# Performance work log

Measured on AMD Instinct MI355X. Metric: run time of the kernel, lower is better.

## Reference

```python
import jax, jax.numpy as jnp
import numpy as np

B, T, N, F = 8, 32, 10000, 16
E = 160000
HG, HT = 64, 128
EPS = 1e-5


def setup_inputs() -> dict:
    key = jax.random.key(0)
    ks = jax.random.split(key, 12)
    s = lambda i, shape, sc=0.05: jax.random.normal(ks[i], shape, dtype=jnp.float32) * sc
    return {
        "x_seq": jax.random.normal(ks[0], (B, T, N, F), dtype=jnp.float32),
        "edge_index": jax.random.randint(ks[1], (2, E), 0, N),
        "W1l": s(2, (HG, F)), "b1": jnp.zeros((HG,), jnp.float32), "W1r": s(3, (HG, F)),
        "g1": jnp.ones((HG,), jnp.float32), "be1": jnp.zeros((HG,), jnp.float32),
        "W2l": s(4, (HG, HG)), "b2": jnp.zeros((HG,), jnp.float32), "W2r": s(5, (HG, HG)),
        "g2": jnp.ones((HG,), jnp.float32), "be2": jnp.zeros((HG,), jnp.float32),
        "W_ih": s(6, (3 * HT, HG)), "W_hh": s(7, (3 * HT, HT)),
        "b_ih": jnp.zeros((3 * HT,), jnp.float32), "b_hh": jnp.zeros((3 * HT,), jnp.float32),
        "Wh": s(8, (1, HT)), "bh": jnp.zeros((1,), jnp.float32),
    }


def _layernorm(h, g, b):
    mu = h.mean(-1, keepdims=True)
    var = ((h - mu) ** 2).mean(-1, keepdims=True)
    return (h - mu) * jax.lax.rsqrt(var + EPS) * g + b


def reference(x_seq, edge_index, W1l, b1, W1r, g1, be1, W2l, b2, W2r, g2, be2,
              W_ih, W_hh, b_ih, b_hh, Wh, bh):
    src, dst = edge_index[0], edge_index[1]
    deg = jax.ops.segment_sum(jnp.ones((E,), x_seq.dtype), dst, num_segments=N)
    inv_deg = (1.0 / jnp.maximum(deg, 1.0))[:, None]  # [N,1]

    def aggregate(x):  # x: [B,N,F] -> mean over incoming neighbors per node
        msgs = x[:, src, :]  # [B,E,F] gather
        agg = jax.vmap(lambda m: jax.ops.segment_sum(m, dst, num_segments=N))(msgs)
        return agg * inv_deg

    def sage(x, Wl, bl, Wr, g, b):
        # PyG SAGEConv(mean): lin_l(agg) + lin_r(x); then LayerNorm + ReLU (dropout=eval)
        h = aggregate(x) @ Wl.T + bl + x @ Wr.T
        return jax.nn.relu(_layernorm(h, g, b))

    def step(_, xt):  # xt: [B,N,F] -> pooled [B,HG]
        h = sage(xt, W1l, b1, W1r, g1, be1)
        h = sage(h, W2l, b2, W2r, g2, be2)
        return None, h.mean(axis=1)

    _, H = jax.lax.scan(step, None, jnp.swapaxes(x_seq, 0, 1))  # [T,B,HG]

    def gru_step(h, x):  # PyTorch GRU gate order: r, z, n
        gi = x @ W_ih.T + b_ih
        gh = h @ W_hh.T + b_hh
        ir, iz, in_ = jnp.split(gi, 3, axis=-1)
        hr, hz, hn = jnp.split(gh, 3, axis=-1)
        r = jax.nn.sigmoid(ir + hr)
        z = jax.nn.sigmoid(iz + hz)
        n = jnp.tanh(in_ + r * hn)
        return (1.0 - z) * n + z * h, None

    h0 = jnp.zeros((x_seq.shape[0], HT), x_seq.dtype)
    ht, _ = jax.lax.scan(gru_step, h0, H)
    return (ht @ Wh.T + bh).squeeze(-1)  # [B]
```

## Files before the change

kernel.cpp:

```cpp
#include <hip/hip_runtime.h>
#include <math.h>

#define B_ 8
#define T_ 32
#define N_ 10000
#define F_ 16
#define E_ 160000
#define HG_ 64
#define HT_ 128
#define BT_ (B_*T_)
#define PB_ 157
#define EPS_ 1e-5f

typedef __attribute__((ext_vector_type(8))) short bf16x8_t;
typedef __attribute__((ext_vector_type(4))) float f32x4_t;
typedef __attribute__((ext_vector_type(2))) float f32x2_t;

__device__ inline unsigned short f2bf(float f) {
  unsigned u = __float_as_uint(f);
  u += 0x7fffu + ((u >> 16) & 1u);
  return (unsigned short)(u >> 16);
}
__device__ inline unsigned pack2bf(float a, float b) {
  return (unsigned)f2bf(a) | ((unsigned)f2bf(b) << 16);
}
__device__ inline void accp(f32x2_t& a, unsigned u) {
  f32x2_t t = { __uint_as_float(u << 16), __uint_as_float(u & 0xffff0000u) };
  a += t;
}
__device__ inline void bfly2(f32x2_t& a, int m) {
  f32x2_t t = { __shfl_xor(a.x, m), __shfl_xor(a.y, m) };
  a += t;
}

__global__ void k_zero(int* p, int n) {
  int i = blockIdx.x * 256 + threadIdx.x;
  if (i < n) p[i] = 0;
}

__global__ void k_deg(const int* __restrict__ dst, int* __restrict__ deg) {
  int e = blockIdx.x * 256 + threadIdx.x;
  if (e < E_) atomicAdd(&deg[dst[e]], 1);
}

__global__ void k_scan(const int* __restrict__ deg, int* __restrict__ row_ptr,
                       float* __restrict__ inv_deg) {
  __shared__ int part[256];
  int tid = threadIdx.x;
  int base = tid * 40;
  int s = 0;
  for (int i = 0; i < 40; i++) { int idx = base + i; if (idx < N_) s += deg[idx]; }
  part[tid] = s;
  __syncthreads();
  if (tid == 0) {
    int run = 0;
    for (int i = 0; i < 256; i++) { int v = part[i]; part[i] = run; run += v; }
  }
  __syncthreads();
  int run = part[tid];
  for (int i = 0; i < 40; i++) {
    int idx = base + i;
    if (idx < N_) {
      row_ptr[idx] = run;
      int d = deg[idx];
      run += d;
      inv_deg[idx] = 1.0f / fmaxf((float)d, 1.0f);
    } else if (idx == N_) {
      row_ptr[N_] = run;
    }
  }
}

__global__ void k_fill(const int* __restrict__ src, const int* __restrict__ dst,
                       const int* __restrict__ row_ptr, int* __restrict__ cursor,
                       int* __restrict__ col) {
  int e = blockIdx.x * 256 + threadIdx.x;
  if (e < E_) {
    int d = dst[e];
    int p = atomicAdd(&cursor[d], 1);
    col[row_ptr[d] + p] = src[e];
  }
}

__global__ void k_prepw(const float* __restrict__ W2l, const float* __restrict__ W2r,
                        unsigned short* __restrict__ Wbf) {
  int idx = blockIdx.x * 256 + threadIdx.x;
  if (idx >= 4 * 4 * 64 * 8) return;
  int q  = idx & 7;
  int l  = (idx >> 3) & 63;
  int ks = (idx >> 9) & 3;
  int w  = idx >> 11;
  int j = w * 16 + (l & 15);
  int k = ks * 32 + ((l >> 4) * 8) + q;
  float v = (k < 64) ? W2l[j * 64 + k] : W2r[j * 64 + (k - 64)];
  Wbf[idx] = f2bf(v);
}

__global__ void k_prepw1(const float* __restrict__ W1l, const float* __restrict__ W1r,
                         float* __restrict__ Wt1) {
  int idx = blockIdx.x * 256 + threadIdx.x;
  if (idx >= 4 * 32 * 16) return;
  int w = idx >> 9;
  int r = idx & 511;
  int k = r >> 4;
  int jj = r & 15;
  int j = w * 16 + jj;
  float v = (k < 16) ? W1l[j * 16 + k] : W1r[j * 16 + (k - 16)];
  Wt1[idx] = v;
}

__launch_bounds__(256, 8)
__global__ void k_sage1t(const float* __restrict__ x, const int* __restrict__ row_ptr,
                         const int* __restrict__ col, const float* __restrict__ inv_deg,
                         const float* __restrict__ Wt1, const float* __restrict__ b1,
                         const float* __restrict__ g1, const float* __restrict__ be1,
                         unsigned short* __restrict__ h1, const float* __restrict__ zrow,
                         int bt0, int CH, int swz) {
  __shared__ float Z1[64 * 36];
  __shared__ float red[2][4][64];
  int i = blockIdx.x;
  int btl, chunk;
  if (swz) {
    int xcd = i & 7; int j = i >> 3; int per = CH >> 3;
    btl = xcd * per + j / PB_; chunk = j % PB_;
  } else {
    btl = i / PB_; chunk = i % PB_;
  }
  int bt = bt0 + btl;
  size_t xbase = (size_t)bt * (N_ * F_);
  int tid = threadIdx.x;
  int w = __builtin_amdgcn_readfirstlane(tid >> 6);
  int lane = tid & 63;
  int n0 = chunk * 64;
  int node = lane >> 4;
  int eo2 = (lane >> 2) & 3;
  int fq2 = lane & 3;
  const float4* x4b = (const float4*)(x + xbase);
  const float4* z4 = (const float4*)zrow;

  for (int p = 0; p < 4; ++p) {
    int mA = w * 16 + p * 4;
    int nA = n0 + mA;
    int s0A = 0, dA = 0, s0B = 0, dB = 0, s0C = 0, dC = 0, s0D = 0, dD = 0;
    float ivA = 0.f, ivB = 0.f, ivC = 0.f, ivD = 0.f;
    if (nA < N_)     { s0A = row_ptr[nA];   dA = row_ptr[nA+1] - s0A; ivA = inv_deg[nA]; }
    if (nA+1 < N_)   { s0B = row_ptr[nA+1]; dB = row_ptr[nA+2] - s0B; ivB = inv_deg[nA+1]; }
    if (nA+2 < N_)   { s0C = row_ptr[nA+2]; dC = row_ptr[nA+3] - s0C; ivC = inv_deg[nA+2]; }
    if (nA+3 < N_)   { s0D = row_ptr[nA+3]; dD = row_ptr[nA+4] - s0D; ivD = inv_deg[nA+3]; }
    int s0My = node < 2 ? (node ? s0B : s0A) : (node == 2 ? s0C : s0D);
    int dMy  = node < 2 ? (node ? dB  : dA)  : (node == 2 ? dC  : dD);
    float ivMy = node < 2 ? (node ? ivB : ivA) : (node == 2 ? ivC : ivD);
    int dcMy = dMy > 64 ? 64 : dMy;
    int dcA = dA > 64 ? 64 : dA, dcB = dB > 64 ? 64 : dB;
    int dcC = dC > 64 ? 64 : dC, dcD = dD > 64 ? 64 : dD;
    int mx = max(max(dcA, dcB), max(dcC, dcD));
    int rounds = (mx + 3) >> 2;
    int pos = lane & 15;
    int c0r = (pos      < dMy) ? col[s0My + pos]      : 0;
    int c1r = (pos + 16 < dMy) ? col[s0My + pos + 16] : 0;
    int c2r = (pos + 32 < dMy) ? col[s0My + pos + 32] : 0;
    int c3r = (pos + 48 < dMy) ? col[s0My + pos + 48] : 0;
    float4 a = {0.f, 0.f, 0.f, 0.f};
    int r = 0;
#define S1BODY(REG, BASE)                                             \
    {                                                                 \
      int idx = eo2 + 4 * r;                                          \
      int s = __shfl(REG, (lane & 48) | (idx - BASE));                \
      const float4* bp = (idx < dcMy) ? (x4b + (size_t)s * 4) : z4;   \
      float4 v = bp[fq2];                                             \
      a.x += v.x; a.y += v.y; a.z += v.z; a.w += v.w;                 \
    }
    for (; r < rounds && r < 4; ++r)  S1BODY(c0r, 0)
    for (; r < rounds && r < 8; ++r)  S1BODY(c1r, 16)
    for (; r < rounds && r < 12; ++r) S1BODY(c2r, 32)
    for (; r < rounds; ++r)           S1BODY(c3r, 48)
#undef S1BODY
    if (dMy > 64) {
      for (int e = s0My + 64; e < s0My + dMy; ++e) {
        if (eo2 == 0) {
          float4 v = x4b[(size_t)col[e] * 4 + fq2];
          a.x += v.x; a.y += v.y; a.z += v.z; a.w += v.w;
        }
      }
    }
    a.x += __shfl_xor(a.x, 4);  a.y += __shfl_xor(a.y, 4);
    a.z += __shfl_xor(a.z, 4);  a.w += __shfl_xor(a.w, 4);
    a.x += __shfl_xor(a.x, 8);  a.y += __shfl_xor(a.y, 8);
    a.z += __shfl_xor(a.z, 8);  a.w += __shfl_xor(a.w, 8);
    if (eo2 == 0) {
      float4 w4;
      w4.x = a.x * ivMy; w4.y = a.y * ivMy; w4.z = a.z * ivMy; w4.w = a.w * ivMy;
      *(float4*)&Z1[(mA + node) * 36 + fq2 * 4] = w4;
    } else if (eo2 == 1) {
      int nS = nA + node;
      float4 sv = {0.f, 0.f, 0.f, 0.f};
      if (nS < N_) sv = x4b[(size_t)nS * 4 + fq2];
      *(float4*)&Z1[(mA + node) * 36 + 16 + fq2 * 4] = sv;
    }
  }
  __syncthreads();

  int m = lane;
  const float* wp0 = Wt1 + w * 512;
  float acc[16];
#pragma unroll
  for (int jj = 0; jj < 16; ++jj) acc[jj] = b1[w * 16 + jj];
  const float* zrw = Z1 + m * 36;
#pragma unroll 4
  for (int k = 0; k < 32; ++k) {
    float z = zrw[k];
    const float* wp = wp0 + k * 16;
#pragma unroll
    for (int jj = 0; jj < 16; ++jj) acc[jj] = fmaf(z, wp[jj], acc[jj]);
  }

  float s1 = 0.f, s2 = 0.f;
#pragma unroll
  for (int jj = 0; jj < 16; ++jj) { s1 += acc[jj]; s2 += acc[jj] * acc[jj]; }
  red[0][w][m] = s1;
  red[1][w][m] = s2;
  __syncthreads();
  float mu = (red[0][0][m] + red[0][1][m] + red[0][2][m] + red[0][3][m]) * (1.f / 64.f);
  float ex2 = (red[1][0][m] + red[1][1][m] + red[1][2][m] + red[1][3][m]) * (1.f / 64.f);
  float var = fmaxf(ex2 - mu * mu, 0.f);
  float rs = rsqrtf(var + EPS_);

  if ((n0 + m) < N_) {
#pragma unroll
    for (int jj = 0; jj < 16; ++jj)
      acc[jj] = fmaxf((acc[jj] - mu) * rs * g1[w * 16 + jj] + be1[w * 16 + jj], 0.f);
    uint4 pa, pb;
    pa.x = pack2bf(acc[0], acc[1]);  pa.y = pack2bf(acc[2], acc[3]);
    pa.z = pack2bf(acc[4], acc[5]);  pa.w = pack2bf(acc[6], acc[7]);
    pb.x = pack2bf(acc[8], acc[9]);  pb.y = pack2bf(acc[10], acc[11]);
    pb.z = pack2bf(acc[12], acc[13]); pb.w = pack2bf(acc[14], acc[15]);
    unsigned short* dst = h1 + ((size_t)btl * N_ + n0 + m) * HG_ + w * 16;
    *(uint4*)dst = pa;
    *(uint4*)(dst + 8) = pb;
  }
}

__launch_bounds__(256, 8)
__global__ void k_sage2t(const unsigned short* __restrict__ h1, const int* __restrict__ row_ptr,
                         const int* __restrict__ col, const float* __restrict__ inv_deg,
                         const unsigned short* __restrict__ Wbf, const float* __restrict__ b2,
                         const float* __restrict__ g2, const float* __restrict__ be2,
                         float* __restrict__ Hsum, const float* __restrict__ zrow,
                         int bt0, int CH, int swz) {
  __shared__ __align__(16) unsigned short Zb[64 * 136];
  __shared__ float red[2][4][64];
  float* Zf = (float*)Zb;
  int i = blockIdx.x;
  int btl, chunk;
  if (swz) {
    int xcd = i & 7; int j = i >> 3; int per = CH >> 3;
    btl = xcd * per + j / PB_; chunk = j % PB_;
  } else {
    btl = i / PB_; chunk = i % PB_;
  }
  int bt = bt0 + btl;
  int b = bt / T_, t = bt % T_;
  size_t hbase = (size_t)btl * (N_ * HG_);
  const uint4* h8 = (const uint4*)(h1 + hbase);
  const uint4* z8 = (const uint4*)zrow;
  int tid = threadIdx.x;
  int w = __builtin_amdgcn_readfirstlane(tid >> 6);
  int lane = tid & 63;
  int n0 = chunk * 64;
  int nsel = lane >> 5;
  int eo2 = (lane >> 3) & 3;
  int fq3 = lane & 7;

  for (int p = 0; p < 8; ++p) {
    int mA = w * 16 + p * 2;
    int nA = n0 + mA, nB = nA + 1;
    int s0A = 0, dA = 0, s0B = 0, dB = 0;
    float ivA = 0.f, ivB = 0.f;
    if (nA < N_) { s0A = row_ptr[nA]; dA = row_ptr[nA + 1] - s0A; ivA = inv_deg[nA]; }
    if (nB < N_) { s0B = row_ptr[nB]; dB = row_ptr[nB + 1] - s0B; ivB = inv_deg[nB]; }
    int s0My = nsel ? s0B : s0A;
    int dMy  = nsel ? dB  : dA;
    float ivMy = nsel ? ivB : ivA;
    int dcMy = dMy > 64 ? 64 : dMy;
    int dcA = dA > 64 ? 64 : dA, dcB = dB > 64 ? 64 : dB;
    int mx = max(dcA, dcB);
    int rounds = (mx + 3) >> 2;
    int pos = lane & 31;
    int c0r = (pos      < dMy) ? col[s0My + pos]      : 0;
    int c1r = (pos + 32 < dMy) ? col[s0My + pos + 32] : 0;
    f32x2_t a0 = {0.f, 0.f}, a1 = {0.f, 0.f}, a2 = {0.f, 0.f}, a3 = {0.f, 0.f};
    int r = 0;
#define S2BODY(REG, BASE)                                               \
    {                                                                   \
      int idx = eo2 + 4 * r;                                            \
      int s = __shfl(REG, (lane & 32) | (idx - BASE));                  \
      const uint4* bp = (idx < dcMy) ? (h8 + (size_t)s * 8) : z8;       \
      uint4 v = bp[fq3];                                                \
      accp(a0, v.x); accp(a1, v.y); accp(a2, v.z); accp(a3, v.w);       \
    }
    for (; r < rounds && r < 8; ++r) S2BODY(c0r, 0)
    for (; r < rounds; ++r)          S2BODY(c1r, 32)
#undef S2BODY
    if (dMy > 64) {
      for (int e = s0My + 64; e < s0My + dMy; ++e) {
        if (eo2 == 0) {
          uint4 v = h8[(size_t)col[e] * 8 + fq3];
          accp(a0, v.x); accp(a1, v.y); accp(a2, v.z); accp(a3, v.w);
        }
      }
    }
    bfly2(a0, 8);  bfly2(a1, 8);  bfly2(a2, 8);  bfly2(a3, 8);
    bfly2(a0, 16); bfly2(a1, 16); bfly2(a2, 16); bfly2(a3, 16);
    if (eo2 == 0) {
      uint4 pk;
      pk.x = pack2bf(a0.x * ivMy, a0.y * ivMy);
      pk.y = pack2bf(a1.x * ivMy, a1.y * ivMy);
      pk.z = pack2bf(a2.x * ivMy, a2.y * ivMy);
      pk.w = pack2bf(a3.x * ivMy, a3.y * ivMy);
      *(uint4*)&Zb[(mA + nsel) * 136 + fq3 * 8] = pk;
    } else if (eo2 == 1) {
      int nS = nA + nsel;
      uint4 sv = (nS < N_) ? h8[(size_t)nS * 8 + fq3] : z8[fq3];
      *(uint4*)&Zb[(mA + nsel) * 136 + 64 + fq3 * 8] = sv;
    }
  }
  __syncthreads();

  int g = lane >> 4, c = lane & 15;
  const bf16x8_t* Wb8 = (const bf16x8_t*)Wbf;
  float bj = b2[w * 16 + c];
  f32x4_t accf[4];
#pragma unroll
  for (int mt = 0; mt < 4; ++mt) accf[mt] = (f32x4_t){bj, bj, bj, bj};
#pragma unroll
  for (int ks = 0; ks < 4; ++ks) {
    bf16x8_t bfr = Wb8[(w * 4 + ks) * 64 + lane];
#pragma unroll
    for (int mt = 0; mt < 4; ++mt) {
      const bf16x8_t* ap = (const bf16x8_t*)&Zb[(mt * 16 + c) * 136 + ks * 32 + g * 8];
      accf[mt] = __builtin_amdgcn_mfma_f32_16x16x32_bf16(*ap, bfr, accf[mt], 0, 0, 0);
    }
  }
  __syncthreads();

#pragma unroll
  for (int mt = 0; mt < 4; ++mt) {
#pragma unroll
    for (int q = 0; q < 4; ++q) {
      int nodeq = mt * 16 + g * 4 + q;
      Zf[nodeq * 68 + w * 16 + c] = accf[mt][q];
    }
  }
  __syncthreads();

  int m = lane;
  float* zr = Zf + m * 68 + w * 16;
  float4 z0 = *(const float4*)(zr + 0);
  float4 z1 = *(const float4*)(zr + 4);
  float4 z2 = *(const float4*)(zr + 8);
  float4 z3 = *(const float4*)(zr + 12);
  float acc[16];
  acc[0] = z0.x; acc[1] = z0.y; acc[2] = z0.z; acc[3] = z0.w;
  acc[4] = z1.x; acc[5] = z1.y; acc[6] = z1.z; acc[7] = z1.w;
  acc[8] = z2.x; acc[9] = z2.y; acc[10] = z2.z; acc[11] = z2.w;
  acc[12] = z3.x; acc[13] = z3.y; acc[14] = z3.z; acc[15] = z3.w;

  float s1 = 0.f, s2 = 0.f;
#pragma unroll
  for (int jj = 0; jj < 16; ++jj) { s1 += acc[jj]; s2 += acc[jj] * acc[jj]; }
  red[0][w][m] = s1;
  red[1][w][m] = s2;
  __syncthreads();
  float mu = (red[0][0][m] + red[0][1][m] + red[0][2][m] + red[0][3][m]) * (1.f / 64.f);
  float ex2 = (red[1][0][m] + red[1][1][m] + red[1][2][m] + red[1][3][m]) * (1.f / 64.f);
  float var = fmaxf(ex2 - mu * mu, 0.f);
  float rs = rsqrtf(var + EPS_);

  bool okm = (n0 + m) < N_;
#pragma unroll
  for (int jj = 0; jj < 16; ++jj) {
    float hv = fmaxf((acc[jj] - mu) * rs * g2[w * 16 + jj] + be2[w * 16 + jj], 0.f);
    acc[jj] = okm ? hv : 0.f;
  }
  float4 o0 = {acc[0], acc[1], acc[2], acc[3]};
  float4 o1 = {acc[4], acc[5], acc[6], acc[7]};
  float4 o2 = {acc[8], acc[9], acc[10], acc[11]};
  float4 o3 = {acc[12], acc[13], acc[14], acc[15]};
  *(float4*)(zr + 0) = o0;  *(float4*)(zr + 4) = o1;
  *(float4*)(zr + 8) = o2;  *(float4*)(zr + 12) = o3;
  __syncthreads();

  float cs = 0.f;
#pragma unroll
  for (int ii = 0; ii < 16; ++ii) cs += Zf[(w * 16 + ii) * 68 + lane];
  red[0][w][lane] = cs;
  __syncthreads();
  if (w == 0) {
    float tot = red[0][0][lane] + red[0][1][lane] + red[0][2][lane] + red[0][3][lane];
    atomicAdd(&Hsum[(t * B_ + b) * HG_ + lane], tot);
  }
}

__global__ void k_gi(const float* __restrict__ Hsum, const float* __restrict__ W_ih,
                     const float* __restrict__ b_ih, float* __restrict__ GI) {
  __shared__ float xv[64];
  int tb = blockIdx.x;
  int tid = threadIdx.x;
  if (tid < 64) xv[tid] = Hsum[tb * 64 + tid] * (1.0f / (float)N_);
  __syncthreads();
  float g = b_ih[tid];
  const float4* W4 = (const float4*)(W_ih + tid * 64);
  const float4* x4 = (const float4*)xv;
#pragma unroll
  for (int q = 0; q < 16; q++) {
    float4 w = W4[q], xq = x4[q];
    g = fmaf(xq.x, w.x, g); g = fmaf(xq.y, w.y, g);
    g = fmaf(xq.z, w.z, g); g = fmaf(xq.w, w.w, g);
  }
  GI[tb * 384 + tid] = g;
}

__global__ void k_gru(const float* __restrict__ GI, const float* __restrict__ W_hh,
                      const float* __restrict__ b_hh, const float* __restrict__ Wh,
                      const float* __restrict__ bh, float* __restrict__ out) {
  __shared__ float hL[128];
  __shared__ float ghL[384];
  __shared__ float red[128];
  int b = blockIdx.x, tid = threadIdx.x;
  if (tid < 128) hL[tid] = 0.f;
  float bhh = b_hh[tid];
  const float4* W4 = (const float4*)(W_hh + tid * 128);
  for (int t = 0; t < T_; ++t) {
    __syncthreads();
    float g = bhh;
    const float4* h4 = (const float4*)hL;
#pragma unroll
    for (int q = 0; q < 32; q++) {
      float4 w = W4[q], hv = h4[q];
      g = fmaf(hv.x, w.x, g); g = fmaf(hv.y, w.y, g);
      g = fmaf(hv.z, w.z, g); g = fmaf(hv.w, w.w, g);
    }
    ghL[tid] = g;
    __syncthreads();
    float hnew = 0.f;
    if (tid < 128) {
      const float* gi = GI + (t * B_ + b) * 384;
      float rr = 1.f / (1.f + expf(-(gi[tid] + ghL[tid])));
      float zz = 1.f / (1.f + expf(-(gi[128 + tid] + ghL[128 + tid])));
      float nn = tanhf(gi[256 + tid] + rr * ghL[256 + tid]);
      hnew = (1.f - zz) * nn + zz * hL[tid];
    }
    __syncthreads();
    if (tid < 128) hL[tid] = hnew;
  }
  __syncthreads();
  if (tid < 128) red[tid] = hL[tid] * Wh[tid];
  __syncthreads();
  if (tid == 0) {
    float s = bh[0];
    for (int k = 0; k < 128; k++) s += red[k];
    out[b] = s;
  }
}

extern "C" void kernel_launch(void* const* d_in, const int* in_sizes, int n_in,
                              void* d_out, int out_size, void* d_ws, size_t ws_size,
                              hipStream_t stream) {
  const float* x    = (const float*)d_in[0];
  const int*   ei   = (const int*)d_in[1];
  const float* W1l  = (const float*)d_in[2];
  const float* b1   = (const float*)d_in[3];
  const float* W1r  = (const float*)d_in[4];
  const float* g1   = (const float*)d_in[5];
  const float* be1  = (const float*)d_in[6];
  const float* W2l  = (const float*)d_in[7];
  const float* b2   = (const float*)d_in[8];
  const float* W2r  = (const float*)d_in[9];
  const float* g2   = (const float*)d_in[10];
  const float* be2  = (const float*)d_in[11];
  const float* W_ih = (const float*)d_in[12];
  const float* W_hh = (const float*)d_in[13];
  const float* b_ih = (const float*)d_in[14];
  const float* b_hh = (const float*)d_in[15];
  const float* Wh   = (const float*)d_in[16];
  const float* bh   = (const float*)d_in[17];
  float* out = (float*)d_out;

  char* ws = (char*)d_ws;
  size_t off = 0;
  auto alloc = [&](size_t bytes) { void* p = ws + off; off += (bytes + 255) & ~(size_t)255; return p; };
  int*   deg     = (int*)alloc((size_t)N_ * 4);
  int*   row_ptr = (int*)alloc((size_t)(N_ + 1) * 4);
  int*   cursor  = (int*)alloc((size_t)N_ * 4);
  int*   col     = (int*)alloc((size_t)E_ * 4);
  float* ivd     = (float*)alloc((size_t)N_ * 4);
  float* Hsum    = (float*)alloc((size_t)BT_ * HG_ * 4);
  float* GI      = (float*)alloc((size_t)BT_ * 384 * 4);
  unsigned short* Wbf = (unsigned short*)alloc((size_t)4 * 4 * 64 * 8 * 2);
  float* Wt1     = (float*)alloc((size_t)4 * 32 * 16 * 4);
  float* zrowp   = (float*)alloc(256);
  size_t fixed = off;
  unsigned short* h1 = (unsigned short*)(ws + off);

  size_t cap = (ws_size > fixed) ? (ws_size - fixed) : 0;
  int CH = (int)(cap / ((size_t)N_ * HG_ * 2));
  if (CH > 64) CH = 64;
  if (CH >= 8) CH &= ~7;
  if (CH < 1) CH = 1;

  int zn = (int)(fixed / 4);
  k_zero<<<(zn + 255) / 256, 256, 0, stream>>>((int*)ws, zn);

  const int* srcp = ei;
  const int* dstp = ei + E_;
  k_deg<<<(E_ + 255) / 256, 256, 0, stream>>>(dstp, deg);
  k_scan<<<1, 256, 0, stream>>>(deg, row_ptr, ivd);
  k_fill<<<(E_ + 255) / 256, 256, 0, stream>>>(srcp, dstp, row_ptr, cursor, col);
  k_prepw<<<32, 256, 0, stream>>>(W2l, W2r, Wbf);
  k_prepw1<<<8, 256, 0, stream>>>(W1l, W1r, Wt1);

  for (int bt0 = 0; bt0 < BT_; bt0 += CH) {
    int c = BT_ - bt0 < CH ? BT_ - bt0 : CH;
    int swz = (c % 8 == 0) ? 1 : 0;
    k_sage1t<<<c * PB_, 256, 0, stream>>>(x, row_ptr, col, ivd, Wt1, b1, g1, be1,
                                          h1, zrowp, bt0, c, swz);
    k_sage2t<<<c * PB_, 256, 0, stream>>>(h1, row_ptr, col, ivd, Wbf, b2, g2, be2,
                                          Hsum, zrowp, bt0, c, swz);
  }
  k_gi<<<BT_, 384, 0, stream>>>(Hsum, W_ih, b_ih, GI);
  k_gru<<<B_, 384, 0, stream>>>(GI, W_hh, b_hh, Wh, bh, out);
}
```

Measured before the change: 1.365 ms.

## Use bf16 MFMA for layer-1 SAGE linear and add zero sentinel row

Layer-1 SAGE now packs the aggregated and self features into bf16 in shared memory and runs the 32x64 projection as a single bf16 MFMA per tile instead of scalar FP32 FMAs. The h1 buffer gains an extra all-zero sentinel row per timestep, so layer-2 gathers can point padded lanes at that row and drop the per-load conditional pointer select; gather addressing switches to 32-bit byte offsets. pack2bf uses the HIP bf16x2 intrinsic. This reduces VALU work and branch overhead, at the cost of layer-1 precision loss from bf16 inputs and a slightly larger h1 buffer.

```diff
diff --git a/kernel.cpp b/kernel.cpp
--- a/kernel.cpp
+++ b/kernel.cpp
@@ -1,4 +1,5 @@
 #include <hip/hip_runtime.h>
+#include <hip/hip_bf16.h>
 #include <math.h>
 
 #define B_ 8
@@ -11,6 +12,7 @@
 #define BT_ (B_*T_)
 #define PB_ 157
 #define EPS_ 1e-5f
+#define NR_ (N_+1)
 
 typedef __attribute__((ext_vector_type(8))) short bf16x8_t;
 typedef __attribute__((ext_vector_type(4))) float f32x4_t;
@@ -22,7 +24,10 @@
   return (unsigned short)(u >> 16);
 }
 __device__ inline unsigned pack2bf(float a, float b) {
-  return (unsigned)f2bf(a) | ((unsigned)f2bf(b) << 16);
+  __hip_bfloat162 h2 = __float22bfloat162_rn(float2{a, b});
+  unsigned u;
+  __builtin_memcpy(&u, &h2, 4);
+  return u;
 }
 __device__ inline void accp(f32x2_t& a, unsigned u) {
   f32x2_t t = { __uint_as_float(u << 16), __uint_as_float(u & 0xffff0000u) };
@@ -97,27 +102,29 @@
 }
 
 __global__ void k_prepw1(const float* __restrict__ W1l, const float* __restrict__ W1r,
-                         float* __restrict__ Wt1) {
+                         unsigned short* __restrict__ Wb1) {
   int idx = blockIdx.x * 256 + threadIdx.x;
-  if (idx >= 4 * 32 * 16) return;
+  if (idx >= 4 * 64 * 8) return;
+  int q = idx & 7;
+  int l = (idx >> 3) & 63;
   int w = idx >> 9;
-  int r = idx & 511;
-  int k = r >> 4;
-  int jj = r & 15;
-  int j = w * 16 + jj;
+  int j = w * 16 + (l & 15);
+  int k = ((l >> 4) * 8) + q;
   float v = (k < 16) ? W1l[j * 16 + k] : W1r[j * 16 + (k - 16)];
-  Wt1[idx] = v;
+  Wb1[idx] = f2bf(v);
 }
 
 __launch_bounds__(256, 8)
 __global__ void k_sage1t(const float* __restrict__ x, const int* __restrict__ row_ptr,
                          const int* __restrict__ col, const float* __restrict__ inv_deg,
-                         const float* __restrict__ Wt1, const float* __restrict__ b1,
+                         const unsigned short* __restrict__ Wb1, const float* __restrict__ b1,
                          const float* __restrict__ g1, const float* __restrict__ be1,
                          unsigned short* __restrict__ h1, const float* __restrict__ zrow,
                          int bt0, int CH, int swz) {
-  __shared__ float Z1[64 * 36];
+  __shared__ __align__(16) unsigned short ZU[64 * 136];
   __shared__ float red[2][4][64];
+  unsigned short* Z1b = ZU;
+  float* Zf = (float*)ZU;
   int i = blockIdx.x;
   int btl, chunk;
   if (swz) {
@@ -188,31 +195,56 @@
     a.x += __shfl_xor(a.x, 8);  a.y += __shfl_xor(a.y, 8);
     a.z += __shfl_xor(a.z, 8);  a.w += __shfl_xor(a.w, 8);
     if (eo2 == 0) {
-      float4 w4;
-      w4.x = a.x * ivMy; w4.y = a.y * ivMy; w4.z = a.z * ivMy; w4.w = a.w * ivMy;
-      *(float4*)&Z1[(mA + node) * 36 + fq2 * 4] = w4;
+      uint2 pk;
+      pk.x = pack2bf(a.x * ivMy, a.y * ivMy);
+      pk.y = pack2bf(a.z * ivMy, a.w * ivMy);
+      *(uint2*)&Z1b[(mA + node) * 40 + fq2 * 4] = pk;
     } else if (eo2 == 1) {
       int nS = nA + node;
       float4 sv = {0.f, 0.f, 0.f, 0.f};
       if (nS < N_) sv = x4b[(size_t)nS * 4 + fq2];
-      *(float4*)&Z1[(mA + node) * 36 + 16 + fq2 * 4] = sv;
+      uint2 pk;
+      pk.x = pack2bf(sv.x, sv.y);
+      pk.y = pack2bf(sv.z, sv.w);
+      *(uint2*)&Z1b[(mA + node) * 40 + 16 + fq2 * 4] = pk;
+    }
+  }
+  __syncthreads();
+
+  int g = lane >> 4, c = lane & 15;
+  float bj = b1[w * 16 + c];
+  f32x4_t accf[4];
+#pragma unroll
+  for (int mt = 0; mt < 4; ++mt) accf[mt] = (f32x4_t){bj, bj, bj, bj};
+  bf16x8_t bfr = ((const bf16x8_t*)Wb1)[w * 64 + lane];
+#pragma unroll
+  for (int mt = 0; mt < 4; ++mt) {
+    const bf16x8_t* ap = (const bf16x8_t*)&Z1b[(mt * 16 + c) * 40 + g * 8];
+    accf[mt] = __builtin_amdgcn_mfma_f32_16x16x32_bf16(*ap, bfr, accf[mt], 0, 0, 0);
+  }
+  __syncthreads();
+
+#pragma unroll
+  for (int mt = 0; mt < 4; ++mt) {
+#pragma unroll
+    for (int q = 0; q < 4; ++q) {
+      int nodeq = mt * 16 + g * 4 + q;
+      Zf[nodeq * 68 + w * 16 + c] = accf[mt][q];
     }
   }
   __syncthreads();
 
   int m = lane;
-  const float* wp0 = Wt1 + w * 512;
+  const float* zr = Zf + m * 68 + w * 16;
+  float4 z0 = *(const float4*)(zr + 0);
+  float4 z1 = *(const float4*)(zr + 4);
+  float4 z2 = *(const float4*)(zr + 8);
+  float4 z3 = *(const float4*)(zr + 12);
   float acc[16];
-#pragma unroll
-  for (int jj = 0; jj < 16; ++jj) acc[jj] = b1[w * 16 + jj];
-  const float* zrw = Z1 + m * 36;
-#pragma unroll 4
-  for (int k = 0; k < 32; ++k) {
-    float z = zrw[k];
-    const float* wp = wp0 + k * 16;
-#pragma unroll
-    for (int jj = 0; jj < 16; ++jj) acc[jj] = fmaf(z, wp[jj], acc[jj]);
-  }
+  acc[0] = z0.x; acc[1] = z0.y; acc[2] = z0.z; acc[3] = z0.w;
+  acc[4] = z1.x; acc[5] = z1.y; acc[6] = z1.z; acc[7] = z1.w;
+  acc[8] = z2.x; acc[9] = z2.y; acc[10] = z2.z; acc[11] = z2.w;
+  acc[12] = z3.x; acc[13] = z3.y; acc[14] = z3.z; acc[15] = z3.w;
 
   float s1 = 0.f, s2 = 0.f;
 #pragma unroll
@@ -225,7 +257,9 @@
   float var = fmaxf(ex2 - mu * mu, 0.f);
   float rs = rsqrtf(var + EPS_);
 
-  if ((n0 + m) < N_) {
+  int nAbs = n0 + m;
+  unsigned short* dst = h1 + ((size_t)btl * NR_ + nAbs) * HG_ + w * 16;
+  if (nAbs < N_) {
 #pragma unroll
     for (int jj = 0; jj < 16; ++jj)
       acc[jj] = fmaxf((acc[jj] - mu) * rs * g1[w * 16 + jj] + be1[w * 16 + jj], 0.f);
@@ -234,9 +268,12 @@
     pa.z = pack2bf(acc[4], acc[5]);  pa.w = pack2bf(acc[6], acc[7]);
     pb.x = pack2bf(acc[8], acc[9]);  pb.y = pack2bf(acc[10], acc[11]);
     pb.z = pack2bf(acc[12], acc[13]); pb.w = pack2bf(acc[14], acc[15]);
-    unsigned short* dst = h1 + ((size_t)btl * N_ + n0 + m) * HG_ + w * 16;
     *(uint4*)dst = pa;
     *(uint4*)(dst + 8) = pb;
+  } else if (nAbs == N_) {
+    uint4 zz = {0, 0, 0, 0};
+    *(uint4*)dst = zz;
+    *(uint4*)(dst + 8) = zz;
   }
 }
 
@@ -245,8 +282,7 @@
                          const int* __restrict__ col, const float* __restrict__ inv_deg,
                          const unsigned short* __restrict__ Wbf, const float* __restrict__ b2,
                          const float* __restrict__ g2, const float* __restrict__ be2,
-                         float* __restrict__ Hsum, const float* __restrict__ zrow,
-                         int bt0, int CH, int swz) {
+                         float* __restrict__ Hsum, int bt0, int CH, int swz) {
   __shared__ __align__(16) unsigned short Zb[64 * 136];
   __shared__ float red[2][4][64];
   float* Zf = (float*)Zb;
@@ -260,9 +296,7 @@
   }
   int bt = bt0 + btl;
   int b = bt / T_, t = bt % T_;
-  size_t hbase = (size_t)btl * (N_ * HG_);
-  const uint4* h8 = (const uint4*)(h1 + hbase);
-  const uint4* z8 = (const uint4*)zrow;
+  const char* h8c = (const char*)(h1 + (size_t)btl * (NR_ * HG_));
   int tid = threadIdx.x;
   int w = __builtin_amdgcn_readfirstlane(tid >> 6);
   int lane = tid & 63;
@@ -270,6 +304,7 @@
   int nsel = lane >> 5;
   int eo2 = (lane >> 3) & 3;
   int fq3 = lane & 7;
+  unsigned foff = (unsigned)fq3 * 16;
 
   for (int p = 0; p < 8; ++p) {
     int mA = w * 16 + p * 2;
@@ -281,21 +316,19 @@
     int s0My = nsel ? s0B : s0A;
     int dMy  = nsel ? dB  : dA;
     float ivMy = nsel ? ivB : ivA;
-    int dcMy = dMy > 64 ? 64 : dMy;
     int dcA = dA > 64 ? 64 : dA, dcB = dB > 64 ? 64 : dB;
     int mx = max(dcA, dcB);
     int rounds = (mx + 3) >> 2;
     int pos = lane & 31;
-    int c0r = (pos      < dMy) ? col[s0My + pos]      : 0;
-    int c1r = (pos + 32 < dMy) ? col[s0My + pos + 32] : 0;
+    int c0r = (pos      < dMy) ? col[s0My + pos]      : N_;
+    int c1r = (pos + 32 < dMy) ? col[s0My + pos + 32] : N_;
     f32x2_t a0 = {0.f, 0.f}, a1 = {0.f, 0.f}, a2 = {0.f, 0.f}, a3 = {0.f, 0.f};
     int r = 0;
 #define S2BODY(REG, BASE)                                               \
     {                                                                   \
       int idx = eo2 + 4 * r;                                            \
       int s = __shfl(REG, (lane & 32) | (idx - BASE));                  \
-      const uint4* bp = (idx < dcMy) ? (h8 + (size_t)s * 8) : z8;       \
-      uint4 v = bp[fq3];                                                \
+      uint4 v = *(const uint4*)(h8c + (((unsigned)s << 7) + foff));     \
       accp(a0, v.x); accp(a1, v.y); accp(a2, v.z); accp(a3, v.w);       \
     }
     for (; r < rounds && r < 8; ++r) S2BODY(c0r, 0)
@@ -304,7 +337,7 @@
     if (dMy > 64) {
       for (int e = s0My + 64; e < s0My + dMy; ++e) {
         if (eo2 == 0) {
-          uint4 v = h8[(size_t)col[e] * 8 + fq3];
+          uint4 v = *(const uint4*)(h8c + (((unsigned)col[e] << 7) + foff));
           accp(a0, v.x); accp(a1, v.y); accp(a2, v.z); accp(a3, v.w);
         }
       }
@@ -320,7 +353,8 @@
       *(uint4*)&Zb[(mA + nsel) * 136 + fq3 * 8] = pk;
     } else if (eo2 == 1) {
       int nS = nA + nsel;
-      uint4 sv = (nS < N_) ? h8[(size_t)nS * 8 + fq3] : z8[fq3];
+      int nSc = nS < N_ ? nS : N_;
+      uint4 sv = *(const uint4*)(h8c + (((unsigned)nSc << 7) + foff));
       *(uint4*)&Zb[(mA + nsel) * 136 + 64 + fq3 * 8] = sv;
     }
   }
@@ -497,13 +531,13 @@
   float* Hsum    = (float*)alloc((size_t)BT_ * HG_ * 4);
   float* GI      = (float*)alloc((size_t)BT_ * 384 * 4);
   unsigned short* Wbf = (unsigned short*)alloc((size_t)4 * 4 * 64 * 8 * 2);
-  float* Wt1     = (float*)alloc((size_t)4 * 32 * 16 * 4);
+  unsigned short* Wb1 = (unsigned short*)alloc((size_t)4 * 64 * 8 * 2);
   float* zrowp   = (float*)alloc(256);
   size_t fixed = off;
   unsigned short* h1 = (unsigned short*)(ws + off);
 
   size_t cap = (ws_size > fixed) ? (ws_size - fixed) : 0;
-  int CH = (int)(cap / ((size_t)N_ * HG_ * 2));
+  int CH = (int)(cap / ((size_t)NR_ * HG_ * 2));
   if (CH > 64) CH = 64;
   if (CH >= 8) CH &= ~7;
   if (CH < 1) CH = 1;
@@ -517,15 +551,15 @@
   k_scan<<<1, 256, 0, stream>>>(deg, row_ptr, ivd);
   k_fill<<<(E_ + 255) / 256, 256, 0, stream>>>(srcp, dstp, row_ptr, cursor, col);
   k_prepw<<<32, 256, 0, stream>>>(W2l, W2r, Wbf);
-  k_prepw1<<<8, 256, 0, stream>>>(W1l, W1r, Wt1);
+  k_prepw1<<<8, 256, 0, stream>>>(W1l, W1r, Wb1);
 
   for (int bt0 = 0; bt0 < BT_; bt0 += CH) {
     int c = BT_ - bt0 < CH ? BT_ - bt0 : CH;
     int swz = (c % 8 == 0) ? 1 : 0;
-    k_sage1t<<<c * PB_, 256, 0, stream>>>(x, row_ptr, col, ivd, Wt1, b1, g1, be1,
+    k_sage1t<<<c * PB_, 256, 0, stream>>>(x, row_ptr, col, ivd, Wb1, b1, g1, be1,
                                           h1, zrowp, bt0, c, swz);
     k_sage2t<<<c * PB_, 256, 0, stream>>>(h1, row_ptr, col, ivd, Wbf, b2, g2, be2,
-                                          Hsum, zrowp, bt0, c, swz);
+                                          Hsum, bt0, c, swz);
   }
   k_gi<<<BT_, 384, 0, stream>>>(Hsum, W_ih, b_ih, GI);
   k_gru<<<B_, 384, 0, stream>>>(GI, W_hh, b_hh, Wh, bh, out);
```

Measured after the change: 1.303 ms. 1.05x faster.
